# Performance work log

Measured on AMD Instinct MI355X. Metric: run time of the kernel, lower is better.

## Reference

```python
import jax, jax.numpy as jnp
import numpy as np

B, S, D, H = 4, 2048, 1024, 16
DH = D // H  # 64


def setup_inputs() -> dict:
    key = jax.random.key(0)
    ks = jax.random.split(key, 7)
    scale = 1.0 / np.sqrt(DH)  # ~ torch Linear init scale
    return {
        "seqs": jax.random.normal(ks[0], (B, S, D), dtype=jnp.float32),
        "Wq": jax.random.normal(ks[1], (H, DH, DH), dtype=jnp.float32) * scale,
        "bq": jax.random.normal(ks[2], (H, DH), dtype=jnp.float32) * scale,
        "Wk": jax.random.normal(ks[3], (H, DH, DH), dtype=jnp.float32) * scale,
        "bk": jax.random.normal(ks[4], (H, DH), dtype=jnp.float32) * scale,
        "Wv": jax.random.normal(ks[5], (H, DH, DH), dtype=jnp.float32) * scale,
        "bv": jax.random.normal(ks[6], (H, DH), dtype=jnp.float32) * scale,
    }


def reference(seqs, Wq, bq, Wk, bk, Wv, bv):
    # seqs: [B, S, D] -> per-head slices [B, S, H, DH]
    x = seqs.reshape(B, S, H, DH)
    # torch Linear: y = s @ W.T + b  (W: [out, in]) -> einsum over 'in' axis d
    q = jnp.einsum("bshd,hed->bshe", x, Wq) + bq  # [B,S,H,DH]
    k = jnp.einsum("bshd,hed->bshe", x, Wk) + bk
    v = jnp.einsum("bshd,hed->bshe", x, Wv) + bv
    inv_sqrt = 1.0 / jnp.sqrt(jnp.asarray(DH, dtype=seqs.dtype))
    scores = jnp.einsum("bshe,bthe->bhst", q, k) * inv_sqrt  # [B,H,S,S]
    attn = jax.nn.softmax(scores, axis=-1)
    out = jnp.einsum("bhst,bthe->bshe", attn, v)  # [B,S,H,DH]
    # torch.hstack over heads == concat along feature dim
    return out.reshape(B, S, D)
```

## Files before the change

kernel.cpp:

```cpp
#include <hip/hip_runtime.h>
#include <hip/hip_bf16.h>

#define NB 4
#define NS 2048
#define ND 1024
#define NH 16
#define NDH 64
#define SCF 0.18033688011112042f

typedef __attribute__((ext_vector_type(8))) short bf16x8;
typedef __attribute__((ext_vector_type(4))) float f32x4;

__device__ __forceinline__ float bf2f(unsigned short u) {
    union { unsigned int u; float f; } x; x.u = ((unsigned int)u) << 16; return x.f;
}
__device__ __forceinline__ unsigned short f2bf(float f) {
    union { float f; unsigned int u; } x; x.f = f;
    unsigned int r = x.u + 0x7FFFu + ((x.u >> 16) & 1u);
    return (unsigned short)(r >> 16);
}
__device__ __forceinline__ unsigned short f2bf_fast(float f) {
    union { float f; unsigned int u; } x; x.f = f;
    return (unsigned short)((x.u + 0x8000u) >> 16);
}
__device__ __forceinline__ unsigned int pkbf(float a, float b) {
    union { float f; unsigned int u; } x, y; x.f = a; y.f = b;
    return __builtin_amdgcn_perm(y.u + 0x8000u, x.u + 0x8000u, 0x07060302u);
}
__device__ __forceinline__ unsigned int pktr(float a, float b) {
    union { float f; unsigned int u; } x, y; x.f = a; y.f = b;
    return __builtin_amdgcn_perm(y.u, x.u, 0x07060302u);
}

__device__ __forceinline__ int detect_f32(const unsigned short* x, int tid,
                                          int* sflag)
{
    if (tid < 64) {
        int bad = 0, zer = 0;
        for (int i = tid; i < 1024; i += 64) {
            const unsigned short u = x[2 * i];
            const int e = (u >> 7) & 0xFF;
            if (e >= 0x8F) bad++;
            if (e == 0 && (u & 0x7F)) bad++;
            if (u == 0) zer++;
        }
        #pragma unroll
        for (int off = 1; off < 64; off <<= 1) {
            bad += __shfl_xor(bad, off, 64);
            zer += __shfl_xor(zer, off, 64);
        }
        if (tid == 0) *sflag = (bad > 64 || zer > 512) ? 1 : 0;
    }
    __syncthreads();
    return *sflag;
}

__global__ __launch_bounds__(256) void qkv_proj_kernel(
    const unsigned short* __restrict__ x,
    const void* __restrict__ Wq, const void* __restrict__ bq,
    const void* __restrict__ Wk, const void* __restrict__ bk,
    const void* __restrict__ Wv, const void* __restrict__ bv,
    unsigned short* __restrict__ Qw, unsigned short* __restrict__ Kw,
    unsigned short* __restrict__ VwT)
{
    __shared__ __align__(16) unsigned short Tl[3 * 64 * 72];
    __shared__ int sflag;

    const int tid  = threadIdx.x;
    const int isf32 = detect_f32(x, tid, &sflag);
    const int wave = tid >> 6, lane = tid & 63;
    const int quad = lane >> 4, l16 = lane & 15;
    const int ttile = blockIdx.x, h = blockIdx.y;
    const int b  = ttile >> 5;
    const int s0 = (ttile & 31) * 64;
    const int bh = b * NH + h;

    const int tok_a = ttile * 64 + wave * 16 + l16;
    bf16x8 af0, af1;
    if (isf32) {
        const f32x4* xp = (const f32x4*)((const float*)x + (size_t)tok_a * ND + h * NDH);
        const f32x4 v0 = xp[quad * 2], v1 = xp[quad * 2 + 1];
        const f32x4 v2 = xp[8 + quad * 2], v3 = xp[8 + quad * 2 + 1];
        union { bf16x8 v; unsigned int d[4]; } a0, a1;
        a0.d[0] = pkbf(v0[0], v0[1]); a0.d[1] = pkbf(v0[2], v0[3]);
        a0.d[2] = pkbf(v1[0], v1[1]); a0.d[3] = pkbf(v1[2], v1[3]);
        a1.d[0] = pkbf(v2[0], v2[1]); a1.d[1] = pkbf(v2[2], v2[3]);
        a1.d[2] = pkbf(v3[0], v3[1]); a1.d[3] = pkbf(v3[2], v3[3]);
        af0 = a0.v; af1 = a1.v;
    } else {
        const unsigned short* xr = x + (size_t)tok_a * ND + h * NDH;
        af0 = *(const bf16x8*)(xr + quad * 8);
        af1 = *(const bf16x8*)(xr + 32 + quad * 8);
    }

    const void* Wsrc[3] = { Wq, Wk, Wv };
    const void* Bsrc[3] = { bq, bk, bv };

    #pragma unroll
    for (int m = 0; m < 3; ++m) {
        unsigned short* R = Tl + m * (64 * 72);
        #pragma unroll
        for (int n = 0; n < 4; ++n) {
            bf16x8 b0, b1;
            if (isf32) {
                const float* wrow = (const float*)Wsrc[m] + h * 4096
                                    + (n * 16 + l16) * NDH;
                const f32x4* wp = (const f32x4*)wrow;
                f32x4 w0 = wp[quad * 2], w1 = wp[quad * 2 + 1];
                f32x4 w2 = wp[8 + quad * 2], w3 = wp[8 + quad * 2 + 1];
                if (m == 0) {
                    #pragma unroll
                    for (int j = 0; j < 4; ++j) {
                        w0[j] *= SCF; w1[j] *= SCF; w2[j] *= SCF; w3[j] *= SCF;
                    }
                }
                union { bf16x8 v; unsigned int d[4]; } t0, t1;
                t0.d[0] = pkbf(w0[0], w0[1]); t0.d[1] = pkbf(w0[2], w0[3]);
                t0.d[2] = pkbf(w1[0], w1[1]); t0.d[3] = pkbf(w1[2], w1[3]);
                t1.d[0] = pkbf(w2[0], w2[1]); t1.d[1] = pkbf(w2[2], w2[3]);
                t1.d[2] = pkbf(w3[0], w3[1]); t1.d[3] = pkbf(w3[2], w3[3]);
                b0 = t0.v; b1 = t1.v;
            } else {
                const unsigned short* wrow = (const unsigned short*)Wsrc[m]
                                             + h * 4096 + (n * 16 + l16) * NDH;
                b0 = *(const bf16x8*)(wrow + quad * 8);
                b1 = *(const bf16x8*)(wrow + 32 + quad * 8);
                if (m == 0) {
                    #pragma unroll
                    for (int j = 0; j < 8; ++j) {
                        b0[j] = (short)f2bf(bf2f((unsigned short)b0[j]) * SCF);
                        b1[j] = (short)f2bf(bf2f((unsigned short)b1[j]) * SCF);
                    }
                }
            }
            f32x4 acc = {0.f, 0.f, 0.f, 0.f};
            acc = __builtin_amdgcn_mfma_f32_16x16x32_bf16(af0, b0, acc, 0, 0, 0);
            acc = __builtin_amdgcn_mfma_f32_16x16x32_bf16(af1, b1, acc, 0, 0, 0);
            float bias = isf32 ? ((const float*)Bsrc[m])[h * NDH + n * 16 + l16]
                               : bf2f(((const unsigned short*)Bsrc[m])[h * NDH + n * 16 + l16]);
            if (m == 0) bias *= SCF;
            if (m < 2) {
                #pragma unroll
                for (int r = 0; r < 4; ++r) {
                    const int row = wave * 16 + quad * 4 + r;
                    R[row * 72 + n * 16 + l16] = f2bf_fast(acc[r] + bias);
                }
            } else {
                #pragma unroll
                for (int r = 0; r < 4; ++r) {
                    const int tok = wave * 16 + quad * 4 + r;
                    const int pc = ((tok & 15) << 2) | (tok >> 4);
                    R[(n * 16 + l16) * 72 + pc] = f2bf_fast(acc[r] + bias);
                }
            }
        }
    }
    __syncthreads();
    #pragma unroll
    for (int p = 0; p < 2; ++p) {
        const int ch = tid + p * 256;
        const int tl = ch >> 3, sub = ch & 7;
        *(bf16x8*)(Qw + ((size_t)bh * NS + s0 + tl) * NDH + sub * 8) =
            *(const bf16x8*)(Tl + tl * 72 + sub * 8);
        *(bf16x8*)(Kw + ((size_t)bh * NS + s0 + tl) * NDH + sub * 8) =
            *(const bf16x8*)(Tl + 64 * 72 + tl * 72 + sub * 8);
        *(bf16x8*)(VwT + ((size_t)bh * NDH + tl) * NS + s0 + sub * 8) =
            *(const bf16x8*)(Tl + 2 * 64 * 72 + tl * 72 + sub * 8);
    }
}

__global__ __launch_bounds__(256, 2) void attn_kernel(
    const unsigned short* __restrict__ xdet,
    const unsigned short* __restrict__ Qw,
    const unsigned short* __restrict__ Kw,
    const unsigned short* __restrict__ VwT,
    unsigned short* __restrict__ out)
{
    __shared__ __align__(16) unsigned short smem[8 * 64 * 72];
    __shared__ int sflag;
    unsigned short* Pt = smem + 4 * 64 * 72;
    unsigned short* Ot = smem;

    const int tid  = threadIdx.x;
    const int isf32 = detect_f32(xdet, tid, &sflag);
    const int wave = tid >> 6, lane = tid & 63;
    const int quad = lane >> 4, l16 = lane & 15;
    const int qt = blockIdx.x & 7;
    const int bh = blockIdx.x >> 3;
    const int b = bh >> 4, h = bh & 15;

    const unsigned short* Qb = Qw  + (size_t)bh * NS * NDH;
    const unsigned short* Kb = Kw  + (size_t)bh * NS * NDH;
    const unsigned short* Vb = VwT + (size_t)bh * NDH * NS;

    bf16x8 qf[4][2];
    #pragma unroll
    for (int mh = 0; mh < 4; ++mh) {
        const int tok = qt * 256 + wave * 64 + mh * 16 + l16;
        qf[mh][0] = *(const bf16x8*)(Qb + (size_t)tok * NDH + quad * 8);
        qf[mh][1] = *(const bf16x8*)(Qb + (size_t)tok * NDH + 32 + quad * 8);
    }

    bf16x8 ones_b;
    {
        const short v = (l16 == 0) ? (short)0x3F80 : (short)0;
        #pragma unroll
        for (int j = 0; j < 8; ++j) ones_b[j] = v;
    }

    f32x4 o[4][4], os[4];
    #pragma unroll
    for (int mh = 0; mh < 4; ++mh) {
        #pragma unroll
        for (int n = 0; n < 4; ++n) o[mh][n] = f32x4{0.f, 0.f, 0.f, 0.f};
        os[mh] = f32x4{0.f, 0.f, 0.f, 0.f};
    }

    const int stage_r = tid >> 3, stage_c = tid & 7;
    unsigned short* PtW = Pt + wave * (64 * 72);

    bf16x8 kpre[2], vpre[2];
    #pragma unroll
    for (int p = 0; p < 2; ++p) {
        const int rr = stage_r + p * 32;
        kpre[p] = *(const bf16x8*)(Kb + (size_t)rr * NDH + stage_c * 8);
        vpre[p] = *(const bf16x8*)(Vb + (size_t)rr * NS + stage_c * 8);
    }

    for (int kt = 0; kt < NS / 64; ++kt) {
        unsigned short* KB = smem + (kt & 1) * (64 * 72);
        unsigned short* VB = smem + (2 + (kt & 1)) * (64 * 72);
        #pragma unroll
        for (int p = 0; p < 2; ++p) {
            const int rr = stage_r + p * 32;
            *(bf16x8*)(KB + rr * 72 + stage_c * 8) = kpre[p];
            *(bf16x8*)(VB + rr * 72 + stage_c * 8) = vpre[p];
        }
        __syncthreads();
        if (kt + 1 < NS / 64) {
            #pragma unroll
            for (int p = 0; p < 2; ++p) {
                const int rr = stage_r + p * 32;
                kpre[p] = *(const bf16x8*)(Kb + (size_t)((kt + 1) * 64 + rr) * NDH + stage_c * 8);
                vpre[p] = *(const bf16x8*)(Vb + (size_t)rr * NS + (kt + 1) * 64 + stage_c * 8);
            }
        }

        bf16x8 kb[4][2];
        #pragma unroll
        for (int n = 0; n < 4; ++n) {
            kb[n][0] = *(const bf16x8*)(KB + (n * 16 + l16) * 72 + quad * 8);
            kb[n][1] = *(const bf16x8*)(KB + (n * 16 + l16) * 72 + 32 + quad * 8);
        }
        #pragma unroll
        for (int mh = 0; mh < 4; ++mh) {
            f32x4 sf[4];
            #pragma unroll
            for (int n = 0; n < 4; ++n) {
                f32x4 acc = {0.f, 0.f, 0.f, 0.f};
                acc = __builtin_amdgcn_mfma_f32_16x16x32_bf16(qf[mh][0], kb[n][0], acc, 0, 0, 0);
                acc = __builtin_amdgcn_mfma_f32_16x16x32_bf16(qf[mh][1], kb[n][1], acc, 0, 0, 0);
                sf[n] = acc;
            }
            #pragma unroll
            for (int r = 0; r < 4; ++r) {
                const float p0 = __builtin_amdgcn_exp2f(sf[0][r]);
                const float p1 = __builtin_amdgcn_exp2f(sf[1][r]);
                const float p2 = __builtin_amdgcn_exp2f(sf[2][r]);
                const float p3 = __builtin_amdgcn_exp2f(sf[3][r]);
                uint2 d; d.x = pktr(p0, p1); d.y = pktr(p2, p3);
                *(uint2*)(PtW + (mh * 16 + quad * 4 + r) * 72 + l16 * 4) = d;
            }
        }

        bf16x8 vb[4][2];
        #pragma unroll
        for (int n = 0; n < 4; ++n) {
            vb[n][0] = *(const bf16x8*)(VB + (n * 16 + l16) * 72 + quad * 8);
            vb[n][1] = *(const bf16x8*)(VB + (n * 16 + l16) * 72 + 32 + quad * 8);
        }
        #pragma unroll
        for (int mh = 0; mh < 4; ++mh) {
            const bf16x8 pa0 = *(const bf16x8*)(PtW + (mh * 16 + l16) * 72 + quad * 8);
            const bf16x8 pa1 = *(const bf16x8*)(PtW + (mh * 16 + l16) * 72 + 32 + quad * 8);
            #pragma unroll
            for (int n = 0; n < 4; ++n) {
                o[mh][n] = __builtin_amdgcn_mfma_f32_16x16x32_bf16(pa0, vb[n][0], o[mh][n], 0, 0, 0);
                o[mh][n] = __builtin_amdgcn_mfma_f32_16x16x32_bf16(pa1, vb[n][1], o[mh][n], 0, 0, 0);
            }
            os[mh] = __builtin_amdgcn_mfma_f32_16x16x32_bf16(pa0, ones_b, os[mh], 0, 0, 0);
            os[mh] = __builtin_amdgcn_mfma_f32_16x16x32_bf16(pa1, ones_b, os[mh], 0, 0, 0);
        }
    }

    float inv[4][4];
    #pragma unroll
    for (int mh = 0; mh < 4; ++mh)
        #pragma unroll
        for (int r = 0; r < 4; ++r)
            inv[mh][r] = 1.0f / __shfl(os[mh][r], lane & 48, 64);

    if (isf32) {
        float* of = (float*)out;
        #pragma unroll
        for (int mh = 0; mh < 4; ++mh) {
            #pragma unroll
            for (int r = 0; r < 4; ++r) {
                const int s = qt * 256 + wave * 64 + mh * 16 + quad * 4 + r;
                #pragma unroll
                for (int n = 0; n < 4; ++n)
                    of[((size_t)(b * NS + s)) * ND + h * NDH + n * 16 + l16] =
                        o[mh][n][r] * inv[mh][r];
            }
        }
    } else {
        __syncthreads();
        #pragma unroll
        for (int mh = 0; mh < 4; ++mh) {
            #pragma unroll
            for (int r = 0; r < 4; ++r) {
                const int row = wave * 64 + mh * 16 + quad * 4 + r;
                #pragma unroll
                for (int n = 0; n < 4; ++n)
                    Ot[row * 72 + n * 16 + l16] = f2bf(o[mh][n][r] * inv[mh][r]);
            }
        }
        __syncthreads();
        #pragma unroll
        for (int p = 0; p < 8; ++p) {
            const int ch = tid + p * 256;
            const int tl = ch >> 3, sub = ch & 7;
            const int s = qt * 256 + tl;
            *(bf16x8*)(out + ((size_t)(b * NS + s)) * ND + h * NDH + sub * 8) =
                *(const bf16x8*)(Ot + tl * 72 + sub * 8);
        }
    }
}

extern "C" void kernel_launch(void* const* d_in, const int* in_sizes, int n_in,
                              void* d_out, int out_size, void* d_ws, size_t ws_size,
                              hipStream_t stream)
{
    const unsigned short* x = (const unsigned short*)d_in[0];
    const size_t per = (size_t)NB * NH * NS * NDH;
    unsigned short* Qw  = (unsigned short*)d_ws;
    unsigned short* Kw  = Qw + per;
    unsigned short* VwT = Kw + per;

    qkv_proj_kernel<<<dim3(NB * NS / 64, NH), 256, 0, stream>>>(
        x, d_in[1], d_in[2], d_in[3], d_in[4], d_in[5], d_in[6], Qw, Kw, VwT);
    attn_kernel<<<NB * NH * (NS / 256), 256, 0, stream>>>(
        x, Qw, Kw, VwT, (unsigned short*)d_out);
}
```

Before: 221.1 us.

## Precompute bf16 weights once, per-row P·V, scalar row sums, smaller LDS

Adds a small pre-kernel that detects the input dtype once and converts and scales Wq/Wk/Wv and the biases to bf16 in workspace. The projection and attention kernels then read a flag instead of each block re-running detection and conversion. In attention, each 16-row P tile is written to LDS and consumed immediately, shrinking the per-wave P buffer and total shared memory, which may allow more blocks per CU. Softmax row sums are now accumulated in scalar adds plus a shuffle reduction instead of extra ones-vector MFMAs. The cost is an extra kernel launch and some added VALU work.

```diff
diff --git a/kernel.cpp b/kernel.cpp
--- a/kernel.cpp
+++ b/kernel.cpp
@@ -32,9 +32,17 @@
     return __builtin_amdgcn_perm(y.u, x.u, 0x07060302u);
 }
 
-__device__ __forceinline__ int detect_f32(const unsigned short* x, int tid,
-                                          int* sflag)
+__global__ __launch_bounds__(256) void convert_w_kernel(
+    const unsigned short* __restrict__ x,
+    const void* __restrict__ Wq, const void* __restrict__ bq,
+    const void* __restrict__ Wk, const void* __restrict__ bk,
+    const void* __restrict__ Wv, const void* __restrict__ bv,
+    int* __restrict__ flag,
+    unsigned short* __restrict__ Wb,
+    unsigned short* __restrict__ Bb)
 {
+    __shared__ int sflag;
+    const int tid = threadIdx.x;
     if (tid < 64) {
         int bad = 0, zer = 0;
         for (int i = tid; i < 1024; i += 64) {
@@ -49,25 +57,43 @@
             bad += __shfl_xor(bad, off, 64);
             zer += __shfl_xor(zer, off, 64);
         }
-        if (tid == 0) *sflag = (bad > 64 || zer > 512) ? 1 : 0;
+        if (tid == 0) {
+            const int f = (bad > 64 || zer > 512) ? 1 : 0;
+            sflag = f;
+            flag[0] = f;
+        }
     }
     __syncthreads();
-    return *sflag;
+    const int isf32 = sflag;
+
+    const void* Wsrc[3] = { Wq, Wk, Wv };
+    const void* Bsrc[3] = { bq, bk, bv };
+    const int NW = 3 * 65536, NBIAS = 3 * 1024;
+    for (int i = blockIdx.x * blockDim.x + tid; i < NW + NBIAS;
+         i += gridDim.x * blockDim.x) {
+        int m, off; const void* src; unsigned short* dst;
+        if (i < NW) { m = i >> 16; off = i & 65535; src = Wsrc[m]; dst = Wb + i; }
+        else { int j = i - NW; m = j >> 10; off = j & 1023; src = Bsrc[m];
+               dst = Bb + j; }
+        float v = isf32 ? ((const float*)src)[off]
+                        : bf2f(((const unsigned short*)src)[off]);
+        if (m == 0) v *= SCF;
+        *dst = f2bf(v);
+    }
 }
 
 __global__ __launch_bounds__(256) void qkv_proj_kernel(
     const unsigned short* __restrict__ x,
-    const void* __restrict__ Wq, const void* __restrict__ bq,
-    const void* __restrict__ Wk, const void* __restrict__ bk,
-    const void* __restrict__ Wv, const void* __restrict__ bv,
+    const unsigned short* __restrict__ Wb,
+    const unsigned short* __restrict__ Bb,
+    const int* __restrict__ flag,
     unsigned short* __restrict__ Qw, unsigned short* __restrict__ Kw,
     unsigned short* __restrict__ VwT)
 {
     __shared__ __align__(16) unsigned short Tl[3 * 64 * 72];
-    __shared__ int sflag;
-
+
+    const int isf32 = flag[0];
     const int tid  = threadIdx.x;
-    const int isf32 = detect_f32(x, tid, &sflag);
     const int wave = tid >> 6, lane = tid & 63;
     const int quad = lane >> 4, l16 = lane & 15;
     const int ttile = blockIdx.x, h = blockIdx.y;
@@ -93,52 +119,19 @@
         af1 = *(const bf16x8*)(xr + 32 + quad * 8);
     }
 
-    const void* Wsrc[3] = { Wq, Wk, Wv };
-    const void* Bsrc[3] = { bq, bk, bv };
-
     #pragma unroll
     for (int m = 0; m < 3; ++m) {
+        const unsigned short* W = Wb + m * 65536 + h * 4096;
         unsigned short* R = Tl + m * (64 * 72);
         #pragma unroll
         for (int n = 0; n < 4; ++n) {
-            bf16x8 b0, b1;
-            if (isf32) {
-                const float* wrow = (const float*)Wsrc[m] + h * 4096
-                                    + (n * 16 + l16) * NDH;
-                const f32x4* wp = (const f32x4*)wrow;
-                f32x4 w0 = wp[quad * 2], w1 = wp[quad * 2 + 1];
-                f32x4 w2 = wp[8 + quad * 2], w3 = wp[8 + quad * 2 + 1];
-                if (m == 0) {
-                    #pragma unroll
-                    for (int j = 0; j < 4; ++j) {
-                        w0[j] *= SCF; w1[j] *= SCF; w2[j] *= SCF; w3[j] *= SCF;
-                    }
-                }
-                union { bf16x8 v; unsigned int d[4]; } t0, t1;
-                t0.d[0] = pkbf(w0[0], w0[1]); t0.d[1] = pkbf(w0[2], w0[3]);
-                t0.d[2] = pkbf(w1[0], w1[1]); t0.d[3] = pkbf(w1[2], w1[3]);
-                t1.d[0] = pkbf(w2[0], w2[1]); t1.d[1] = pkbf(w2[2], w2[3]);
-                t1.d[2] = pkbf(w3[0], w3[1]); t1.d[3] = pkbf(w3[2], w3[3]);
-                b0 = t0.v; b1 = t1.v;
-            } else {
-                const unsigned short* wrow = (const unsigned short*)Wsrc[m]
-                                             + h * 4096 + (n * 16 + l16) * NDH;
-                b0 = *(const bf16x8*)(wrow + quad * 8);
-                b1 = *(const bf16x8*)(wrow + 32 + quad * 8);
-                if (m == 0) {
-                    #pragma unroll
-                    for (int j = 0; j < 8; ++j) {
-                        b0[j] = (short)f2bf(bf2f((unsigned short)b0[j]) * SCF);
-                        b1[j] = (short)f2bf(bf2f((unsigned short)b1[j]) * SCF);
-                    }
-                }
-            }
+            const unsigned short* wrow = W + (n * 16 + l16) * NDH;
+            const bf16x8 b0 = *(const bf16x8*)(wrow + quad * 8);
+            const bf16x8 b1 = *(const bf16x8*)(wrow + 32 + quad * 8);
             f32x4 acc = {0.f, 0.f, 0.f, 0.f};
             acc = __builtin_amdgcn_mfma_f32_16x16x32_bf16(af0, b0, acc, 0, 0, 0);
             acc = __builtin_amdgcn_mfma_f32_16x16x32_bf16(af1, b1, acc, 0, 0, 0);
-            float bias = isf32 ? ((const float*)Bsrc[m])[h * NDH + n * 16 + l16]
-                               : bf2f(((const unsigned short*)Bsrc[m])[h * NDH + n * 16 + l16]);
-            if (m == 0) bias *= SCF;
+            const float bias = bf2f(Bb[m * 1024 + h * NDH + n * 16 + l16]);
             if (m < 2) {
                 #pragma unroll
                 for (int r = 0; r < 4; ++r) {
@@ -170,19 +163,18 @@
 }
 
 __global__ __launch_bounds__(256, 2) void attn_kernel(
-    const unsigned short* __restrict__ xdet,
     const unsigned short* __restrict__ Qw,
     const unsigned short* __restrict__ Kw,
     const unsigned short* __restrict__ VwT,
+    const int* __restrict__ flag,
     unsigned short* __restrict__ out)
 {
-    __shared__ __align__(16) unsigned short smem[8 * 64 * 72];
-    __shared__ int sflag;
+    __shared__ __align__(16) unsigned short smem[5 * 64 * 72];
     unsigned short* Pt = smem + 4 * 64 * 72;
     unsigned short* Ot = smem;
 
+    const int isf32 = flag[0];
     const int tid  = threadIdx.x;
-    const int isf32 = detect_f32(xdet, tid, &sflag);
     const int wave = tid >> 6, lane = tid & 63;
     const int quad = lane >> 4, l16 = lane & 15;
     const int qt = blockIdx.x & 7;
@@ -201,23 +193,18 @@
         qf[mh][1] = *(const bf16x8*)(Qb + (size_t)tok * NDH + 32 + quad * 8);
     }
 
-    bf16x8 ones_b;
-    {
-        const short v = (l16 == 0) ? (short)0x3F80 : (short)0;
-        #pragma unroll
-        for (int j = 0; j < 8; ++j) ones_b[j] = v;
-    }
-
-    f32x4 o[4][4], os[4];
+    f32x4 o[4][4];
+    float os[4][4];
     #pragma unroll
     for (int mh = 0; mh < 4; ++mh) {
         #pragma unroll
         for (int n = 0; n < 4; ++n) o[mh][n] = f32x4{0.f, 0.f, 0.f, 0.f};
-        os[mh] = f32x4{0.f, 0.f, 0.f, 0.f};
+        #pragma unroll
+        for (int r = 0; r < 4; ++r) os[mh][r] = 0.f;
     }
 
     const int stage_r = tid >> 3, stage_c = tid & 7;
-    unsigned short* PtW = Pt + wave * (64 * 72);
+    unsigned short* PtW = Pt + wave * (16 * 72);
 
     bf16x8 kpre[2], vpre[2];
     #pragma unroll
@@ -246,12 +233,15 @@
             }
         }
 
-        bf16x8 kb[4][2];
+        bf16x8 kb[4][2], vb[4][2];
         #pragma unroll
         for (int n = 0; n < 4; ++n) {
             kb[n][0] = *(const bf16x8*)(KB + (n * 16 + l16) * 72 + quad * 8);
             kb[n][1] = *(const bf16x8*)(KB + (n * 16 + l16) * 72 + 32 + quad * 8);
-        }
+            vb[n][0] = *(const bf16x8*)(VB + (n * 16 + l16) * 72 + quad * 8);
+            vb[n][1] = *(const bf16x8*)(VB + (n * 16 + l16) * 72 + 32 + quad * 8);
+        }
+
         #pragma unroll
         for (int mh = 0; mh < 4; ++mh) {
             f32x4 sf[4];
@@ -268,37 +258,32 @@
                 const float p1 = __builtin_amdgcn_exp2f(sf[1][r]);
                 const float p2 = __builtin_amdgcn_exp2f(sf[2][r]);
                 const float p3 = __builtin_amdgcn_exp2f(sf[3][r]);
+                os[mh][r] += (p0 + p1) + (p2 + p3);
                 uint2 d; d.x = pktr(p0, p1); d.y = pktr(p2, p3);
-                *(uint2*)(PtW + (mh * 16 + quad * 4 + r) * 72 + l16 * 4) = d;
-            }
-        }
-
-        bf16x8 vb[4][2];
-        #pragma unroll
-        for (int n = 0; n < 4; ++n) {
-            vb[n][0] = *(const bf16x8*)(VB + (n * 16 + l16) * 72 + quad * 8);
-            vb[n][1] = *(const bf16x8*)(VB + (n * 16 + l16) * 72 + 32 + quad * 8);
-        }
-        #pragma unroll
-        for (int mh = 0; mh < 4; ++mh) {
-            const bf16x8 pa0 = *(const bf16x8*)(PtW + (mh * 16 + l16) * 72 + quad * 8);
-            const bf16x8 pa1 = *(const bf16x8*)(PtW + (mh * 16 + l16) * 72 + 32 + quad * 8);
+                *(uint2*)(PtW + (quad * 4 + r) * 72 + l16 * 4) = d;
+            }
+            const bf16x8 pa0 = *(const bf16x8*)(PtW + l16 * 72 + quad * 8);
+            const bf16x8 pa1 = *(const bf16x8*)(PtW + l16 * 72 + 32 + quad * 8);
             #pragma unroll
             for (int n = 0; n < 4; ++n) {
                 o[mh][n] = __builtin_amdgcn_mfma_f32_16x16x32_bf16(pa0, vb[n][0], o[mh][n], 0, 0, 0);
                 o[mh][n] = __builtin_amdgcn_mfma_f32_16x16x32_bf16(pa1, vb[n][1], o[mh][n], 0, 0, 0);
             }
-            os[mh] = __builtin_amdgcn_mfma_f32_16x16x32_bf16(pa0, ones_b, os[mh], 0, 0, 0);
-            os[mh] = __builtin_amdgcn_mfma_f32_16x16x32_bf16(pa1, ones_b, os[mh], 0, 0, 0);
         }
     }
 
     float inv[4][4];
     #pragma unroll
-    for (int mh = 0; mh < 4; ++mh)
-        #pragma unroll
-        for (int r = 0; r < 4; ++r)
-            inv[mh][r] = 1.0f / __shfl(os[mh][r], lane & 48, 64);
+    for (int mh = 0; mh < 4; ++mh) {
+        #pragma unroll
+        for (int r = 0; r < 4; ++r) {
+            float s = os[mh][r];
+            #pragma unroll
+            for (int off = 1; off < 16; off <<= 1)
+                s += __shfl_xor(s, off, 64);
+            inv[mh][r] = 1.0f / s;
+        }
+    }
 
     if (isf32) {
         float* of = (float*)out;
@@ -342,13 +327,18 @@
                               hipStream_t stream)
 {
     const unsigned short* x = (const unsigned short*)d_in[0];
+    int* flag = (int*)d_ws;
     const size_t per = (size_t)NB * NH * NS * NDH;
-    unsigned short* Qw  = (unsigned short*)d_ws;
+    unsigned short* Qw  = (unsigned short*)((char*)d_ws + 256);
     unsigned short* Kw  = Qw + per;
     unsigned short* VwT = Kw + per;
-
+    unsigned short* Wb  = VwT + per;
+    unsigned short* Bb  = Wb + 3 * 65536;
+
+    convert_w_kernel<<<256, 256, 0, stream>>>(
+        x, d_in[1], d_in[2], d_in[3], d_in[4], d_in[5], d_in[6], flag, Wb, Bb);
     qkv_proj_kernel<<<dim3(NB * NS / 64, NH), 256, 0, stream>>>(
-        x, d_in[1], d_in[2], d_in[3], d_in[4], d_in[5], d_in[6], Qw, Kw, VwT);
+        x, Wb, Bb, flag, Qw, Kw, VwT);
     attn_kernel<<<NB * NH * (NS / 256), 256, 0, stream>>>(
-        x, Qw, Kw, VwT, (unsigned short*)d_out);
-}
+        Qw, Kw, VwT, flag, (unsigned short*)d_out);
+}
```

Measured after the change: 197.2 us. 10.8% less time.
